# Kernel tuning notes

Measured on AMD Instinct MI355X. Metric: run time of the kernel, lower is better.

The kernel has to match this reference:

```python
import jax, jax.numpy as jnp
import numpy as np

EPS = 1e-5

def group_norm(x, gamma, beta):
    # GroupNorm(num_groups=1) on [N, C]: normalize across channels per row
    mu = jnp.mean(x, axis=-1, keepdims=True)
    var = jnp.mean(jnp.square(x - mu), axis=-1, keepdims=True)
    return (x - mu) * jax.lax.rsqrt(var + EPS) * gamma + beta

def setup_inputs() -> dict:
    key = jax.random.key(0)
    ks = jax.random.split(key, 20)
    Nc, Nt, E, D = 100_000, 100_000, 500_000, 128
    f32 = jnp.float32
    s_in, s_rp, s_ctx = 1.0 / np.sqrt(D), 0.5, 1.0 / np.sqrt(2 * D)
    return {
        "context_feat": jax.random.normal(ks[0], (Nc, D), dtype=f32),
        "target_feat": jax.random.normal(ks[1], (Nt, D), dtype=f32),
        "context_pose": jax.random.normal(ks[2], (Nc, 4), dtype=f32),
        "target_pose": jax.random.normal(ks[3], (Nt, 4), dtype=f32),
        "hi": jax.random.randint(ks[4], (E,), 0, Nc, dtype=jnp.int32),
        "wi": jax.random.randint(ks[5], (E,), 0, Nt, dtype=jnp.int32),
        # params (stored [in, out]; equals torch Linear with transposed weight)
        "W_in": jax.random.normal(ks[6], (D, D), dtype=f32) * s_in,
        "W_rp": jax.random.normal(ks[7], (4, D), dtype=f32) * s_rp,
        "b_rp": jnp.zeros((D,), dtype=f32),
        "W_ctx1": jax.random.normal(ks[8], (2 * D, D), dtype=f32) * s_ctx,
        "g_ctx": jnp.ones((D,), dtype=f32),
        "be_ctx": jnp.zeros((D,), dtype=f32),
        "W_ctx2": jax.random.normal(ks[9], (D, D), dtype=f32) * s_in,
        "g_n": jnp.ones((D,), dtype=f32),
        "be_n": jnp.zeros((D,), dtype=f32),
        "W_m1": jax.random.normal(ks[10], (D, D), dtype=f32) * s_in,
        "g_m1": jnp.ones((D,), dtype=f32),
        "be_m1": jnp.zeros((D,), dtype=f32),
        "W_m2": jax.random.normal(ks[11], (D, D), dtype=f32) * s_in,
        "g_m2": jnp.ones((D,), dtype=f32),
        "be_m2": jnp.zeros((D,), dtype=f32),
    }

def reference(context_feat, target_feat, context_pose, target_pose, hi, wi,
              W_in, W_rp, b_rp, W_ctx1, g_ctx, be_ctx, W_ctx2,
              g_n, be_n, W_m1, g_m1, be_m1, W_m2, g_m2, be_m2):
    # relpose MLP on gathered pose deltas: [E,4] -> [E,128]
    dist_feat = jax.nn.relu((context_pose[hi] - target_pose[wi]) @ W_rp + b_rp)
    # ctx branch: concat gathered context feats with relpose -> [E,256] -> [E,128]
    ctx = jnp.concatenate([context_feat[hi], dist_feat], axis=-1)
    ctx = jax.nn.relu(group_norm(ctx @ W_ctx1, g_ctx, be_ctx)) @ W_ctx2
    # scatter-add onto projected target feats
    identity = target_feat
    tf = target_feat @ W_in
    tf = tf.at[wi].add(ctx)
    tf = jax.nn.relu(group_norm(tf, g_n, be_n))
    # output MLP (Linear+GN+ReLU, Linear+GN)
    tf = jax.nn.relu(group_norm(tf @ W_m1, g_m1, be_m1))
    tf = group_norm(tf @ W_m2, g_m2, be_m2)
    return jax.nn.relu(tf + identity)
```

## Files before the change

### kernel.cpp

```cpp
#include <hip/hip_runtime.h>

typedef __bf16 bf16_t;
typedef bf16_t bf16x4 __attribute__((ext_vector_type(4)));
typedef bf16_t bf16x8 __attribute__((ext_vector_type(8)));
typedef float floatx4 __attribute__((ext_vector_type(4)));

#define EPSF 1e-5f
#define DEV static __device__ __forceinline__

__global__ __launch_bounds__(256) void k_prep(
    const float* __restrict__ W_in, const float* __restrict__ W_ctx1,
    const float* __restrict__ W_ctx2, const float* __restrict__ W_m1,
    const float* __restrict__ W_m2, bf16_t* __restrict__ sw)
{
    int idx = blockIdx.x * 256 + threadIdx.x;
    const float* W; int base, ks;
    if (idx < 16384)      { W = W_in;   base = 0;     ks = 2; }
    else if (idx < 49152) { W = W_ctx1; base = 16384; ks = 3; }
    else if (idx < 65536) { W = W_ctx2; base = 49152; ks = 2; }
    else if (idx < 81920) { W = W_m1;   base = 65536; ks = 2; }
    else                  { W = W_m2;   base = 81920; ks = 2; }
    int local = idx - base;
    int j = local & 7, l = (local >> 3) & 63, rest = local >> 9;
    int s = rest & ((1 << ks) - 1), t = rest >> ks;
    int k = s * 32 + (l >> 4) * 8 + j;
    int n = t * 16 + (l & 15);
    sw[idx] = (bf16_t)W[k * 128 + n];
}

DEV void gn_rows(floatx4* acc, int lane, const float* __restrict__ gamma,
                 const float* __restrict__ beta, bool do_relu)
{
    int m = lane & 15;
    float s1[4] = {0.f,0.f,0.f,0.f}, s2[4] = {0.f,0.f,0.f,0.f};
#pragma unroll
    for (int t = 0; t < 8; ++t)
#pragma unroll
        for (int rr = 0; rr < 4; ++rr) { float v = acc[t][rr]; s1[rr] += v; s2[rr] += v*v; }
#pragma unroll
    for (int mask = 1; mask <= 8; mask <<= 1)
#pragma unroll
        for (int rr = 0; rr < 4; ++rr) {
            s1[rr] += __shfl_xor(s1[rr], mask);
            s2[rr] += __shfl_xor(s2[rr], mask);
        }
    float mean[4], inv[4];
#pragma unroll
    for (int rr = 0; rr < 4; ++rr) {
        mean[rr] = s1[rr] * (1.f/128.f);
        float var = s2[rr] * (1.f/128.f) - mean[rr]*mean[rr];
        inv[rr] = rsqrtf(var + EPSF);
    }
#pragma unroll
    for (int t = 0; t < 8; ++t) {
        int n = t*16 + m;
        float ga = gamma[n], be = beta[n];
#pragma unroll
        for (int rr = 0; rr < 4; ++rr) {
            float v = (acc[t][rr] - mean[rr]) * inv[rr] * ga + be;
            acc[t][rr] = do_relu ? fmaxf(v, 0.f) : v;
        }
    }
}

__global__ __launch_bounds__(256) void k_count(const int* __restrict__ wi,
                                               int* __restrict__ cnt, int E)
{
    int e = blockIdx.x * 256 + threadIdx.x;
    if (e < E) atomicAdd(&cnt[wi[e]], 1);
}

__global__ __launch_bounds__(1024) void k_scan(const int* __restrict__ cnt,
                                               int* __restrict__ off, int Nt)
{
    __shared__ int wsum[16];
    __shared__ int s_carry;
    int tid = threadIdx.x, lane = tid & 63, wid = tid >> 6;
    if (tid == 0) s_carry = 0;
    __syncthreads();
    for (int bs = 0; bs < Nt; bs += 4096) {
        int i0 = bs + tid * 4;
        int v0 = 0, v1 = 0, v2 = 0, v3 = 0;
        if (i0 + 3 < Nt) {
            int4 v = *(const int4*)(cnt + i0);
            v0 = v.x; v1 = v.y; v2 = v.z; v3 = v.w;
        } else {
            if (i0     < Nt) v0 = cnt[i0];
            if (i0 + 1 < Nt) v1 = cnt[i0+1];
            if (i0 + 2 < Nt) v2 = cnt[i0+2];
            if (i0 + 3 < Nt) v3 = cnt[i0+3];
        }
        int tot = v0 + v1 + v2 + v3;
        int x = tot;
#pragma unroll
        for (int d = 1; d < 64; d <<= 1) {
            int y = __shfl_up(x, d);
            if (lane >= d) x += y;
        }
        if (lane == 63) wsum[wid] = x;
        __syncthreads();
        if (wid == 0) {
            int wv = (lane < 16) ? wsum[lane] : 0;
#pragma unroll
            for (int d = 1; d < 16; d <<= 1) {
                int y = __shfl_up(wv, d);
                if (lane >= d) wv += y;
            }
            if (lane < 16) wsum[lane] = wv;
        }
        __syncthreads();
        int ebase = s_carry + ((wid > 0) ? wsum[wid-1] : 0) + (x - tot);
        if (i0 + 3 < Nt) {
            *(int4*)(off + i0) = make_int4(ebase, ebase+v0, ebase+v0+v1, ebase+v0+v1+v2);
        } else {
            if (i0     < Nt) off[i0]   = ebase;
            if (i0 + 1 < Nt) off[i0+1] = ebase + v0;
            if (i0 + 2 < Nt) off[i0+2] = ebase + v0 + v1;
            if (i0 + 3 < Nt) off[i0+3] = ebase + v0 + v1 + v2;
        }
        __syncthreads();
        if (tid == 0) s_carry += wsum[15];
        __syncthreads();
    }
    if (tid == 0) off[Nt] = s_carry;
}

__global__ __launch_bounds__(256) void k_edge5(
    const float* __restrict__ cfeat, const float* __restrict__ cpose,
    const float* __restrict__ tpose, const int* __restrict__ hi,
    const int* __restrict__ wi, const float* __restrict__ W_rp,
    const float* __restrict__ b_rp, const float* __restrict__ g_ctx,
    const float* __restrict__ be_ctx, const bf16_t* __restrict__ swC1,
    const int* __restrict__ off, int* __restrict__ cur,
    bf16_t* __restrict__ hbuf, int E)
{
    __shared__ alignas(16) bf16_t sH[4][2176];
    int tid = threadIdx.x, lane = tid & 63, wave = tid >> 6;
    int tb = (blockIdx.x * 4 + wave) * 16;
    int r = lane & 15, g = lane >> 4;
    int e = min(tb + r, E - 1);
    int ci = hi[e], ti = wi[e];

    floatx4 acc[8];
#pragma unroll
    for (int t = 0; t < 8; ++t) acc[t] = (floatx4){0.f,0.f,0.f,0.f};

    const float4* cf = (const float4*)(cfeat + (size_t)ci * 128);
    float4 p[8];
#pragma unroll
    for (int s = 0; s < 4; ++s) {
        p[2*s]   = cf[s*8 + g*2];
        p[2*s+1] = cf[s*8 + g*2 + 1];
    }

    float4 cp = ((const float4*)cpose)[ci];
    float4 tp = ((const float4*)tpose)[ti];
    float d0 = cp.x - tp.x, d1 = cp.y - tp.y, d2 = cp.z - tp.z, d3 = cp.w - tp.w;
#pragma unroll
    for (int sp = 0; sp < 4; ++sp) {
        int k0 = sp * 32 + g * 8;
        const float4* w0 = (const float4*)(W_rp + k0);
        const float4* w1 = (const float4*)(W_rp + 128 + k0);
        const float4* w2 = (const float4*)(W_rp + 256 + k0);
        const float4* w3 = (const float4*)(W_rp + 384 + k0);
        const float4* bb = (const float4*)(b_rp + k0);
        float o0,o1,o2,o3,o4,o5,o6,o7;
        {
            float4 a0=w0[0], a1=w1[0], a2=w2[0], a3=w3[0], ab=bb[0];
            o0 = fmaxf(d0*a0.x + d1*a1.x + d2*a2.x + d3*a3.x + ab.x, 0.f);
            o1 = fmaxf(d0*a0.y + d1*a1.y + d2*a2.y + d3*a3.y + ab.y, 0.f);
            o2 = fmaxf(d0*a0.z + d1*a1.z + d2*a2.z + d3*a3.z + ab.z, 0.f);
            o3 = fmaxf(d0*a0.w + d1*a1.w + d2*a2.w + d3*a3.w + ab.w, 0.f);
        }
        {
            float4 a0=w0[1], a1=w1[1], a2=w2[1], a3=w3[1], ab=bb[1];
            o4 = fmaxf(d0*a0.x + d1*a1.x + d2*a2.x + d3*a3.x + ab.x, 0.f);
            o5 = fmaxf(d0*a0.y + d1*a1.y + d2*a2.y + d3*a3.y + ab.y, 0.f);
            o6 = fmaxf(d0*a0.z + d1*a1.z + d2*a2.z + d3*a3.z + ab.z, 0.f);
            o7 = fmaxf(d0*a0.w + d1*a1.w + d2*a2.w + d3*a3.w + ab.w, 0.f);
        }
        bf16x8 aF = { (bf16_t)o0, (bf16_t)o1, (bf16_t)o2, (bf16_t)o3,
                      (bf16_t)o4, (bf16_t)o5, (bf16_t)o6, (bf16_t)o7 };
        int s = 4 + sp;
#pragma unroll
        for (int t = 0; t < 8; ++t) {
            bf16x8 bF = *(const bf16x8*)&swC1[(size_t)((t*8 + s)*64 + lane)*8];
            acc[t] = __builtin_amdgcn_mfma_f32_16x16x32_bf16(aF, bF, acc[t], 0, 0, 0);
        }
    }
#pragma unroll
    for (int s = 0; s < 4; ++s) {
        float4 v0 = p[2*s], v1 = p[2*s+1];
        bf16x8 aF = { (bf16_t)v0.x, (bf16_t)v0.y, (bf16_t)v0.z, (bf16_t)v0.w,
                      (bf16_t)v1.x, (bf16_t)v1.y, (bf16_t)v1.z, (bf16_t)v1.w };
#pragma unroll
        for (int t = 0; t < 8; ++t) {
            bf16x8 bF = *(const bf16x8*)&swC1[(size_t)((t*8 + s)*64 + lane)*8];
            acc[t] = __builtin_amdgcn_mfma_f32_16x16x32_bf16(aF, bF, acc[t], 0, 0, 0);
        }
    }
    gn_rows(acc, lane, g_ctx, be_ctx, true);

#pragma unroll
    for (int t = 0; t < 8; ++t)
#pragma unroll
        for (int rr = 0; rr < 4; ++rr)
            sH[wave][(g*4 + rr)*136 + t*16 + r] = (bf16_t)acc[t][rr];

    int r2 = lane >> 2, c2 = lane & 3;
    int e2 = tb + r2;
    bool ev2 = e2 < E;
    int dst = 0;
    if (ev2 && c2 == 0) {
        int t2 = wi[e2];
        dst = off[t2] + atomicAdd(&cur[t2], 1);
    }
    dst = __shfl(dst, lane & ~3);
    if (ev2) {
        bf16_t* hp = hbuf + (size_t)dst * 128 + c2 * 32;
#pragma unroll
        for (int i = 0; i < 4; ++i)
            *(bf16x8*)(hp + i*8) = *(const bf16x8*)&sH[wave][r2*136 + c2*32 + i*8];
    }
}

__global__ __launch_bounds__(256) void k_out3(
    const float* __restrict__ tfeat, const bf16_t* __restrict__ hbuf,
    const int* __restrict__ off,
    const float* __restrict__ g_n, const float* __restrict__ be_n,
    const float* __restrict__ g_m1, const float* __restrict__ be_m1,
    const float* __restrict__ g_m2, const float* __restrict__ be_m2,
    const bf16_t* __restrict__ swIn, const bf16_t* __restrict__ swC2,
    const bf16_t* __restrict__ swM1, const bf16_t* __restrict__ swM2,
    float* __restrict__ out, int Nt)
{
    __shared__ alignas(16) bf16_t sB[4][2176];
    int tid = threadIdx.x, lane = tid & 63, wave = tid >> 6;
    int tb = (blockIdx.x*4 + wave)*16;
    int r = lane & 15, g = lane >> 4;
    int grow = tb + r;
    bool rv = grow < Nt;
    int rclamp = rv ? grow : (Nt - 1);

    const float4* cf = (const float4*)(tfeat + (size_t)rclamp * 128);
    float4 p[8];
#pragma unroll
    for (int s = 0; s < 4; ++s) {
        p[2*s]   = cf[s*8 + g*2];
        p[2*s+1] = cf[s*8 + g*2 + 1];
    }

    float sums[32];
#pragma unroll
    for (int i = 0; i < 32; ++i) sums[i] = 0.f;
    int jb = rv ? off[grow] : 0, je = rv ? off[grow+1] : 0;
    for (int jr = jb; jr < je; ++jr) {
        const bf16_t* hp = hbuf + (size_t)jr*128 + g*8;
#pragma unroll
        for (int s = 0; s < 4; ++s) {
            bf16x8 hv = *(const bf16x8*)(hp + s*32);
#pragma unroll
            for (int q = 0; q < 8; ++q) sums[s*8+q] += (float)hv[q];
        }
    }
#pragma unroll
    for (int s = 0; s < 4; ++s) {
        bf16x8 ah = { (bf16_t)sums[s*8+0], (bf16_t)sums[s*8+1],
                      (bf16_t)sums[s*8+2], (bf16_t)sums[s*8+3],
                      (bf16_t)sums[s*8+4], (bf16_t)sums[s*8+5],
                      (bf16_t)sums[s*8+6], (bf16_t)sums[s*8+7] };
        *(bf16x8*)&sB[wave][r*136 + s*32 + g*8] = ah;
    }

    floatx4 acc[8];
#pragma unroll
    for (int t = 0; t < 8; ++t) acc[t] = (floatx4){0.f,0.f,0.f,0.f};
#pragma unroll
    for (int s = 0; s < 4; ++s) {
        bf16x8 aH = *(const bf16x8*)&sB[wave][r*136 + s*32 + g*8];
#pragma unroll
        for (int t = 0; t < 8; ++t) {
            bf16x8 bF = *(const bf16x8*)&swC2[((t*4+s)*64 + lane)*8];
            acc[t] = __builtin_amdgcn_mfma_f32_16x16x32_bf16(aH, bF, acc[t], 0, 0, 0);
        }
        float4 v0 = p[2*s], v1 = p[2*s+1];
        bf16x8 aF = { (bf16_t)v0.x, (bf16_t)v0.y, (bf16_t)v0.z, (bf16_t)v0.w,
                      (bf16_t)v1.x, (bf16_t)v1.y, (bf16_t)v1.z, (bf16_t)v1.w };
#pragma unroll
        for (int t = 0; t < 8; ++t) {
            bf16x8 bF = *(const bf16x8*)&swIn[((t*4+s)*64 + lane)*8];
            acc[t] = __builtin_amdgcn_mfma_f32_16x16x32_bf16(aF, bF, acc[t], 0, 0, 0);
        }
    }
    gn_rows(acc, lane, g_n, be_n, true);

#pragma unroll
    for (int t = 0; t < 8; ++t)
#pragma unroll
        for (int rr = 0; rr < 4; ++rr)
            sB[wave][(g*4 + rr)*136 + t*16 + r] = (bf16_t)acc[t][rr];
#pragma unroll
    for (int t = 0; t < 8; ++t) acc[t] = (floatx4){0.f,0.f,0.f,0.f};
#pragma unroll
    for (int s = 0; s < 4; ++s) {
        bf16x8 aF = *(const bf16x8*)&sB[wave][r*136 + s*32 + g*8];
#pragma unroll
        for (int t = 0; t < 8; ++t) {
            bf16x8 bF = *(const bf16x8*)&swM1[((t*4+s)*64 + lane)*8];
            acc[t] = __builtin_amdgcn_mfma_f32_16x16x32_bf16(aF, bF, acc[t], 0, 0, 0);
        }
    }
    gn_rows(acc, lane, g_m1, be_m1, true);

#pragma unroll
    for (int t = 0; t < 8; ++t)
#pragma unroll
        for (int rr = 0; rr < 4; ++rr)
            sB[wave][(g*4 + rr)*136 + t*16 + r] = (bf16_t)acc[t][rr];
#pragma unroll
    for (int t = 0; t < 8; ++t) acc[t] = (floatx4){0.f,0.f,0.f,0.f};
#pragma unroll
    for (int s = 0; s < 4; ++s) {
        bf16x8 aF = *(const bf16x8*)&sB[wave][r*136 + s*32 + g*8];
#pragma unroll
        for (int t = 0; t < 8; ++t) {
            bf16x8 bF = *(const bf16x8*)&swM2[((t*4+s)*64 + lane)*8];
            acc[t] = __builtin_amdgcn_mfma_f32_16x16x32_bf16(aF, bF, acc[t], 0, 0, 0);
        }
    }
    gn_rows(acc, lane, g_m2, be_m2, false);

#pragma unroll
    for (int t = 0; t < 8; ++t) {
        int n = t*16 + r;
#pragma unroll
        for (int rr = 0; rr < 4; ++rr) {
            int row = tb + g*4 + rr;
            if (row < Nt) {
                float v = acc[t][rr] + tfeat[(size_t)row*128 + n];
                out[(size_t)row*128 + n] = fmaxf(v, 0.f);
            }
        }
    }
}

__global__ __launch_bounds__(256) void k_gemm_in(
    const float* __restrict__ tfeat, const bf16_t* __restrict__ swW,
    float* __restrict__ tf, int Nt)
{
    __shared__ alignas(16) bf16_t sA[4][2048];
    int tid = threadIdx.x, lane = tid & 63, wave = tid >> 6;

    int tb = (blockIdx.x * 4 + wave) * 16;
    int r = lane >> 2, cb = (lane & 3) * 32;
    int grow = tb + r;
    bool rv = grow < Nt;
    const float4* src = (const float4*)(tfeat + (size_t)(rv ? grow : 0) * 128 + cb);
#pragma unroll
    for (int i = 0; i < 8; ++i) {
        float4 v = rv ? src[i] : make_float4(0.f,0.f,0.f,0.f);
        int k = cb + 4*i;
        int s = k >> 5, q = (k >> 3) & 3, j = k & 7;
        bf16x4 pk = { (bf16_t)v.x, (bf16_t)v.y, (bf16_t)v.z, (bf16_t)v.w };
        *(bf16x4*)&sA[wave][(s*64 + q*16 + r)*8 + j] = pk;
    }
    __syncthreads();
    int m = lane & 15, g = lane >> 4;
    bf16x8 aF[4];
#pragma unroll
    for (int s = 0; s < 4; ++s) aF[s] = *(const bf16x8*)&sA[wave][(s*64 + lane)*8];
#pragma unroll
    for (int t = 0; t < 8; ++t) {
        floatx4 a = {0.f,0.f,0.f,0.f};
#pragma unroll
        for (int s = 0; s < 4; ++s) {
            bf16x8 bF = *(const bf16x8*)&swW[((t*4+s)*64 + lane)*8];
            a = __builtin_amdgcn_mfma_f32_16x16x32_bf16(aF[s], bF, a, 0, 0, 0);
        }
#pragma unroll
        for (int rr = 0; rr < 4; ++rr) {
            int row = tb + g*4 + rr;
            if (row < Nt) tf[(size_t)row*128 + t*16 + m] = a[rr];
        }
    }
}

__global__ __launch_bounds__(256) void k_edge_old(
    const float* __restrict__ cfeat, const float* __restrict__ cpose,
    const float* __restrict__ tpose, const int* __restrict__ hi,
    const int* __restrict__ wi, const float* __restrict__ W_rp,
    const float* __restrict__ b_rp, const float* __restrict__ g_ctx,
    const float* __restrict__ be_ctx, const bf16_t* __restrict__ swC1,
    const bf16_t* __restrict__ swC2, float* __restrict__ tf, int E)
{
    __shared__ alignas(16) bf16_t sA[4][4096];
    int tid = threadIdx.x, lane = tid & 63, wave = tid >> 6;

    int tb = (blockIdx.x * 4 + wave) * 16;
    int r = lane >> 2, cb = (lane & 3) * 32;
    int e = min(tb + r, E - 1);
    int ci = hi[e], ti = wi[e];
    const float4* src = (const float4*)(cfeat + (size_t)ci * 128 + cb);
#pragma unroll
    for (int i = 0; i < 8; ++i) {
        float4 v = src[i];
        int k = cb + 4*i;
        int s = k >> 5, q = (k >> 3) & 3, j = k & 7;
        bf16x4 pk = { (bf16_t)v.x, (bf16_t)v.y, (bf16_t)v.z, (bf16_t)v.w };
        *(bf16x4*)&sA[wave][(s*64 + q*16 + r)*8 + j] = pk;
    }
    float4 cp = ((const float4*)cpose)[ci];
    float4 tp = ((const float4*)tpose)[ti];
    float d0 = cp.x - tp.x, d1 = cp.y - tp.y, d2 = cp.z - tp.z, d3 = cp.w - tp.w;
#pragma unroll
    for (int i = 0; i < 8; ++i) {
        int cc = cb + 4*i;
        float4 w0 = *(const float4*)(W_rp + cc);
        float4 w1 = *(const float4*)(W_rp + 128 + cc);
        float4 w2 = *(const float4*)(W_rp + 256 + cc);
        float4 w3 = *(const float4*)(W_rp + 384 + cc);
        float4 bb = *(const float4*)(b_rp + cc);
        float o0 = fmaxf(d0*w0.x + d1*w1.x + d2*w2.x + d3*w3.x + bb.x, 0.f);
        float o1 = fmaxf(d0*w0.y + d1*w1.y + d2*w2.y + d3*w3.y + bb.y, 0.f);
        float o2 = fmaxf(d0*w0.z + d1*w1.z + d2*w2.z + d3*w3.z + bb.z, 0.f);
        float o3 = fmaxf(d0*w0.w + d1*w1.w + d2*w2.w + d3*w3.w + bb.w, 0.f);
        int k = 128 + cc;
        int s = k >> 5, q = (k >> 3) & 3, j = k & 7;
        bf16x4 pk = { (bf16_t)o0, (bf16_t)o1, (bf16_t)o2, (bf16_t)o3 };
        *(bf16x4*)&sA[wave][(s*64 + q*16 + r)*8 + j] = pk;
    }
    __syncthreads();

    int m = lane & 15, g = lane >> 4;
    bf16x8 aF[8];
#pragma unroll
    for (int s = 0; s < 8; ++s) aF[s] = *(const bf16x8*)&sA[wave][(s*64 + lane)*8];
    floatx4 acc[8];
#pragma unroll
    for (int t = 0; t < 8; ++t) {
        floatx4 a = {0.f,0.f,0.f,0.f};
#pragma unroll
        for (int s = 0; s < 8; ++s) {
            bf16x8 bF = *(const bf16x8*)&swC1[(size_t)((t*8+s)*64 + lane)*8];
            a = __builtin_amdgcn_mfma_f32_16x16x32_bf16(aF[s], bF, a, 0, 0, 0);
        }
        acc[t] = a;
    }
    gn_rows(acc, lane, g_ctx, be_ctx, true);
    __syncthreads();
#pragma unroll
    for (int t = 0; t < 8; ++t) {
        int n = t*16 + m;
        int s = n >> 5, q = (n >> 3) & 3, j = n & 7;
#pragma unroll
        for (int rr = 0; rr < 4; ++rr)
            sA[wave][(s*64 + q*16 + (g*4+rr))*8 + j] = (bf16_t)acc[t][rr];
    }
    __syncthreads();
    bf16x8 aF2[4];
#pragma unroll
    for (int s = 0; s < 4; ++s) aF2[s] = *(const bf16x8*)&sA[wave][(s*64 + lane)*8];
    int dstrow[4]; bool vald[4];
#pragma unroll
    for (int rr = 0; rr < 4; ++rr) {
        int ee = tb + g*4 + rr;
        vald[rr] = ee < E;
        dstrow[rr] = vald[rr] ? wi[ee] : 0;
    }
#pragma unroll
    for (int t = 0; t < 8; ++t) {
        floatx4 a = {0.f,0.f,0.f,0.f};
#pragma unroll
        for (int s = 0; s < 4; ++s) {
            bf16x8 bF = *(const bf16x8*)&swC2[((t*4+s)*64 + lane)*8];
            a = __builtin_amdgcn_mfma_f32_16x16x32_bf16(aF2[s], bF, a, 0, 0, 0);
        }
#pragma unroll
        for (int rr = 0; rr < 4; ++rr) {
            if (vald[rr])
                atomicAdd(&tf[(size_t)dstrow[rr]*128 + t*16 + m], a[rr]);
        }
    }
}

__global__ __launch_bounds__(256) void k_out_old(
    const float* __restrict__ tf, const float* __restrict__ identity,
    const float* __restrict__ g_n, const float* __restrict__ be_n,
    const float* __restrict__ g_m1, const float* __restrict__ be_m1,
    const float* __restrict__ g_m2, const float* __restrict__ be_m2,
    const bf16_t* __restrict__ swM1, const bf16_t* __restrict__ swM2,
    float* __restrict__ out, int Nt)
{
    __shared__ alignas(16) bf16_t sA[4][2048];
    int tid = threadIdx.x, lane = tid & 63, wave = tid >> 6;

    int tb = (blockIdx.x*4 + wave)*16;
    int r = lane >> 2, cb = (lane & 3)*32;
    int grow = tb + r;
    bool rv = grow < Nt;
    const float4* src = (const float4*)(tf + (size_t)(rv ? grow : 0)*128 + cb);
    float vals[32];
    float ls = 0.f, lq = 0.f;
#pragma unroll
    for (int i = 0; i < 8; ++i) {
        float4 v = rv ? src[i] : make_float4(0.f,0.f,0.f,0.f);
        vals[4*i+0]=v.x; vals[4*i+1]=v.y; vals[4*i+2]=v.z; vals[4*i+3]=v.w;
        ls += v.x+v.y+v.z+v.w;
        lq += v.x*v.x+v.y*v.y+v.z*v.z+v.w*v.w;
    }
    ls += __shfl_xor(ls,1); lq += __shfl_xor(lq,1);
    ls += __shfl_xor(ls,2); lq += __shfl_xor(lq,2);
    float mean = ls*(1.f/128.f);
    float inv = rsqrtf(lq*(1.f/128.f) - mean*mean + EPSF);
#pragma unroll
    for (int i = 0; i < 8; ++i) {
        int cc = cb + 4*i;
        float4 ga = *(const float4*)(g_n + cc);
        float4 be = *(const float4*)(be_n + cc);
        float o0 = fmaxf((vals[4*i+0]-mean)*inv*ga.x + be.x, 0.f);
        float o1 = fmaxf((vals[4*i+1]-mean)*inv*ga.y + be.y, 0.f);
        float o2 = fmaxf((vals[4*i+2]-mean)*inv*ga.z + be.z, 0.f);
        float o3 = fmaxf((vals[4*i+3]-mean)*inv*ga.w + be.w, 0.f);
        int s = cc >> 5, q = (cc >> 3) & 3, j = cc & 7;
        bf16x4 pk = { (bf16_t)o0, (bf16_t)o1, (bf16_t)o2, (bf16_t)o3 };
        *(bf16x4*)&sA[wave][(s*64 + q*16 + r)*8 + j] = pk;
    }
    __syncthreads();
    int m = lane & 15, g = lane >> 4;
    bf16x8 aF[4];
#pragma unroll
    for (int s = 0; s < 4; ++s) aF[s] = *(const bf16x8*)&sA[wave][(s*64 + lane)*8];
    floatx4 acc[8];
#pragma unroll
    for (int t = 0; t < 8; ++t) {
        floatx4 a = {0.f,0.f,0.f,0.f};
#pragma unroll
        for (int s = 0; s < 4; ++s) {
            bf16x8 bF = *(const bf16x8*)&swM1[((t*4+s)*64 + lane)*8];
            a = __builtin_amdgcn_mfma_f32_16x16x32_bf16(aF[s], bF, a, 0, 0, 0);
        }
        acc[t] = a;
    }
    gn_rows(acc, lane, g_m1, be_m1, true);
    __syncthreads();
#pragma unroll
    for (int t = 0; t < 8; ++t) {
        int n = t*16 + m;
        int s = n >> 5, q = (n >> 3) & 3, j = n & 7;
#pragma unroll
        for (int rr = 0; rr < 4; ++rr)
            sA[wave][(s*64 + q*16 + (g*4+rr))*8 + j] = (bf16_t)acc[t][rr];
    }
    __syncthreads();
#pragma unroll
    for (int s = 0; s < 4; ++s) aF[s] = *(const bf16x8*)&sA[wave][(s*64 + lane)*8];
#pragma unroll
    for (int t = 0; t < 8; ++t) {
        floatx4 a = {0.f,0.f,0.f,0.f};
#pragma unroll
        for (int s = 0; s < 4; ++s) {
            bf16x8 bF = *(const bf16x8*)&swM2[((t*4+s)*64 + lane)*8];
            a = __builtin_amdgcn_mfma_f32_16x16x32_bf16(aF[s], bF, a, 0, 0, 0);
        }
        acc[t] = a;
    }
    gn_rows(acc, lane, g_m2, be_m2, false);
#pragma unroll
    for (int t = 0; t < 8; ++t) {
        int n = t*16 + m;
#pragma unroll
        for (int rr = 0; rr < 4; ++rr) {
            int row = tb + g*4 + rr;
            if (row < Nt) {
                float v = acc[t][rr] + identity[(size_t)row*128 + n];
                out[(size_t)row*128 + n] = fmaxf(v, 0.f);
            }
        }
    }
}

extern "C" void kernel_launch(void* const* d_in, const int* in_sizes, int n_in,
                              void* d_out, int out_size, void* d_ws, size_t ws_size,
                              hipStream_t stream)
{
    const float* cfeat  = (const float*)d_in[0];
    const float* tfeat  = (const float*)d_in[1];
    const float* cpose  = (const float*)d_in[2];
    const float* tpose  = (const float*)d_in[3];
    const int*   hi     = (const int*)d_in[4];
    const int*   wi     = (const int*)d_in[5];
    const float* W_in   = (const float*)d_in[6];
    const float* W_rp   = (const float*)d_in[7];
    const float* b_rp   = (const float*)d_in[8];
    const float* W_ctx1 = (const float*)d_in[9];
    const float* g_ctx  = (const float*)d_in[10];
    const float* be_ctx = (const float*)d_in[11];
    const float* W_ctx2 = (const float*)d_in[12];
    const float* g_n    = (const float*)d_in[13];
    const float* be_n   = (const float*)d_in[14];
    const float* W_m1   = (const float*)d_in[15];
    const float* g_m1   = (const float*)d_in[16];
    const float* be_m1  = (const float*)d_in[17];
    const float* W_m2   = (const float*)d_in[18];
    const float* g_m2   = (const float*)d_in[19];
    const float* be_m2  = (const float*)d_in[20];

    int Nt = in_sizes[1] / 128;
    int E  = in_sizes[4];
    float* outp = (float*)d_out;

    char* base = (char*)d_ws;
    size_t o = 98304 * sizeof(bf16_t);
    o = (o + 255) & ~(size_t)255;
    size_t o_cnt = o; o += (size_t)Nt * 4;
    o = (o + 255) & ~(size_t)255;
    size_t o_off = o; o += ((size_t)Nt + 1) * 4;
    o = (o + 255) & ~(size_t)255;
    size_t o_cur = o; o += (size_t)Nt * 4;
    o = (o + 255) & ~(size_t)255;
    size_t o_h = o; o += (size_t)E * 128 * sizeof(bf16_t);

    if (ws_size >= o) {
        bf16_t* sw   = (bf16_t*)base;
        int*    cnt  = (int*)(base + o_cnt);
        int*    off  = (int*)(base + o_off);
        int*    cur  = (int*)(base + o_cur);
        bf16_t* hbuf = (bf16_t*)(base + o_h);
        bf16_t* swIn = sw;
        bf16_t* swC1 = sw + 16384;
        bf16_t* swC2 = sw + 49152;
        bf16_t* swM1 = sw + 65536;
        bf16_t* swM2 = sw + 81920;

        hipMemsetAsync(cnt, 0, (size_t)Nt * 4, stream);
        hipMemsetAsync(cur, 0, (size_t)Nt * 4, stream);
        k_prep<<<384, 256, 0, stream>>>(W_in, W_ctx1, W_ctx2, W_m1, W_m2, sw);
        k_count<<<(E + 255) / 256, 256, 0, stream>>>(wi, cnt, E);
        k_scan<<<1, 1024, 0, stream>>>(cnt, off, Nt);
        k_edge5<<<(E + 63) / 64, 256, 0, stream>>>(cfeat, cpose, tpose, hi, wi,
                                                   W_rp, b_rp, g_ctx, be_ctx,
                                                   swC1, off, cur, hbuf, E);
        k_out3<<<(Nt + 63) / 64, 256, 0, stream>>>(tfeat, hbuf, off,
                                                   g_n, be_n, g_m1, be_m1,
                                                   g_m2, be_m2,
                                                   swIn, swC2, swM1, swM2,
                                                   outp, Nt);
    } else {
        float*  tf = (float*)d_ws;
        bf16_t* sw = (bf16_t*)((char*)d_ws + (size_t)Nt * 128 * sizeof(float));
        bf16_t* swIn = sw;
        bf16_t* swC1 = sw + 16384;
        bf16_t* swC2 = sw + 49152;
        bf16_t* swM1 = sw + 65536;
        bf16_t* swM2 = sw + 81920;

        k_prep<<<384, 256, 0, stream>>>(W_in, W_ctx1, W_ctx2, W_m1, W_m2, sw);
        k_gemm_in<<<(Nt + 63) / 64, 256, 0, stream>>>(tfeat, swIn, tf, Nt);
        k_edge_old<<<(E + 63) / 64, 256, 0, stream>>>(cfeat, cpose, tpose, hi, wi,
                                                      W_rp, b_rp, g_ctx, be_ctx,
                                                      swC1, swC2, tf, E);
        k_out_old<<<(Nt + 63) / 64, 256, 0, stream>>>(tf, tfeat, g_n, be_n,
                                                      g_m1, be_m1, g_m2, be_m2,
                                                      swM1, swM2, outp, Nt);
    }
}
```

Before: 485.0 us.

## Process two 16-edge tiles per wave in edge kernel, reusing weight fragments

```diff
diff --git a/kernel.cpp b/kernel.cpp
--- a/kernel.cpp
+++ b/kernel.cpp
@@ -125,7 +125,7 @@
     if (tid == 0) off[Nt] = s_carry;
 }
 
-__global__ __launch_bounds__(256) void k_edge5(
+__global__ __launch_bounds__(256) void k_edge6(
     const float* __restrict__ cfeat, const float* __restrict__ cpose,
     const float* __restrict__ tpose, const int* __restrict__ hi,
     const int* __restrict__ wi, const float* __restrict__ W_rp,
@@ -136,26 +136,45 @@
 {
     __shared__ alignas(16) bf16_t sH[4][2176];
     int tid = threadIdx.x, lane = tid & 63, wave = tid >> 6;
-    int tb = (blockIdx.x * 4 + wave) * 16;
+    int tb = (blockIdx.x * 4 + wave) * 32;
     int r = lane & 15, g = lane >> 4;
-    int e = min(tb + r, E - 1);
-    int ci = hi[e], ti = wi[e];
-
-    floatx4 acc[8];
-#pragma unroll
-    for (int t = 0; t < 8; ++t) acc[t] = (floatx4){0.f,0.f,0.f,0.f};
-
-    const float4* cf = (const float4*)(cfeat + (size_t)ci * 128);
-    float4 p[8];
-#pragma unroll
-    for (int s = 0; s < 4; ++s) {
-        p[2*s]   = cf[s*8 + g*2];
-        p[2*s+1] = cf[s*8 + g*2 + 1];
-    }
-
-    float4 cp = ((const float4*)cpose)[ci];
-    float4 tp = ((const float4*)tpose)[ti];
-    float d0 = cp.x - tp.x, d1 = cp.y - tp.y, d2 = cp.z - tp.z, d3 = cp.w - tp.w;
+    int e0 = min(tb + r, E - 1);
+    int e1 = min(tb + 16 + r, E - 1);
+    int ci0 = hi[e0], ti0 = wi[e0];
+    int ci1 = hi[e1], ti1 = wi[e1];
+
+    int r2 = lane >> 2, c2 = lane & 3;
+    int ea = tb + r2, eb = tb + 16 + r2;
+    bool eva = ea < E, evb = eb < E;
+    int dst0 = 0, dst1 = 0;
+    if (c2 == 0) {
+        if (eva) { int t2 = wi[ea]; dst0 = off[t2] + atomicAdd(&cur[t2], 1); }
+        if (evb) { int t2 = wi[eb]; dst1 = off[t2] + atomicAdd(&cur[t2], 1); }
+    }
+    dst0 = __shfl(dst0, lane & ~3);
+    dst1 = __shfl(dst1, lane & ~3);
+
+    floatx4 acc0[8], acc1[8];
+#pragma unroll
+    for (int t = 0; t < 8; ++t) {
+        acc0[t] = (floatx4){0.f,0.f,0.f,0.f};
+        acc1[t] = (floatx4){0.f,0.f,0.f,0.f};
+    }
+
+    const float4* cf0 = (const float4*)(cfeat + (size_t)ci0 * 128);
+    const float4* cf1 = (const float4*)(cfeat + (size_t)ci1 * 128);
+    float4 t0b[2][2], t1b[2][2];
+    t0b[0][0] = cf0[g*2];     t0b[0][1] = cf0[g*2 + 1];
+    t1b[0][0] = cf1[g*2];     t1b[0][1] = cf1[g*2 + 1];
+    t0b[1][0] = cf0[8 + g*2]; t0b[1][1] = cf0[8 + g*2 + 1];
+    t1b[1][0] = cf1[8 + g*2]; t1b[1][1] = cf1[8 + g*2 + 1];
+
+    float4 cp0 = ((const float4*)cpose)[ci0];
+    float4 tp0 = ((const float4*)tpose)[ti0];
+    float4 cp1 = ((const float4*)cpose)[ci1];
+    float4 tp1 = ((const float4*)tpose)[ti1];
+    float d00 = cp0.x - tp0.x, d01 = cp0.y - tp0.y, d02 = cp0.z - tp0.z, d03 = cp0.w - tp0.w;
+    float d10 = cp1.x - tp1.x, d11 = cp1.y - tp1.y, d12 = cp1.z - tp1.z, d13 = cp1.w - tp1.w;
 #pragma unroll
     for (int sp = 0; sp < 4; ++sp) {
         int k0 = sp * 32 + g * 8;
@@ -164,60 +183,71 @@
         const float4* w2 = (const float4*)(W_rp + 256 + k0);
         const float4* w3 = (const float4*)(W_rp + 384 + k0);
         const float4* bb = (const float4*)(b_rp + k0);
-        float o0,o1,o2,o3,o4,o5,o6,o7;
-        {
-            float4 a0=w0[0], a1=w1[0], a2=w2[0], a3=w3[0], ab=bb[0];
-            o0 = fmaxf(d0*a0.x + d1*a1.x + d2*a2.x + d3*a3.x + ab.x, 0.f);
-            o1 = fmaxf(d0*a0.y + d1*a1.y + d2*a2.y + d3*a3.y + ab.y, 0.f);
-            o2 = fmaxf(d0*a0.z + d1*a1.z + d2*a2.z + d3*a3.z + ab.z, 0.f);
-            o3 = fmaxf(d0*a0.w + d1*a1.w + d2*a2.w + d3*a3.w + ab.w, 0.f);
-        }
-        {
-            float4 a0=w0[1], a1=w1[1], a2=w2[1], a3=w3[1], ab=bb[1];
-            o4 = fmaxf(d0*a0.x + d1*a1.x + d2*a2.x + d3*a3.x + ab.x, 0.f);
-            o5 = fmaxf(d0*a0.y + d1*a1.y + d2*a2.y + d3*a3.y + ab.y, 0.f);
-            o6 = fmaxf(d0*a0.z + d1*a1.z + d2*a2.z + d3*a3.z + ab.z, 0.f);
-            o7 = fmaxf(d0*a0.w + d1*a1.w + d2*a2.w + d3*a3.w + ab.w, 0.f);
-        }
-        bf16x8 aF = { (bf16_t)o0, (bf16_t)o1, (bf16_t)o2, (bf16_t)o3,
-                      (bf16_t)o4, (bf16_t)o5, (bf16_t)o6, (bf16_t)o7 };
+        float o0[8], o1[8];
+#pragma unroll
+        for (int h = 0; h < 2; ++h) {
+            float4 a0 = w0[h], a1 = w1[h], a2 = w2[h], a3 = w3[h], ab = bb[h];
+            o0[4*h+0] = fmaxf(d00*a0.x + d01*a1.x + d02*a2.x + d03*a3.x + ab.x, 0.f);
+            o0[4*h+1] = fmaxf(d00*a0.y + d01*a1.y + d02*a2.y + d03*a3.y + ab.y, 0.f);
+            o0[4*h+2] = fmaxf(d00*a0.z + d01*a1.z + d02*a2.z + d03*a3.z + ab.z, 0.f);
+            o0[4*h+3] = fmaxf(d00*a0.w + d01*a1.w + d02*a2.w + d03*a3.w + ab.w, 0.f);
+            o1[4*h+0] = fmaxf(d10*a0.x + d11*a1.x + d12*a2.x + d13*a3.x + ab.x, 0.f);
+            o1[4*h+1] = fmaxf(d10*a0.y + d11*a1.y + d12*a2.y + d13*a3.y + ab.y, 0.f);
+            o1[4*h+2] = fmaxf(d10*a0.z + d11*a1.z + d12*a2.z + d13*a3.z + ab.z, 0.f);
+            o1[4*h+3] = fmaxf(d10*a0.w + d11*a1.w + d12*a2.w + d13*a3.w + ab.w, 0.f);
+        }
+        bf16x8 aF0 = { (bf16_t)o0[0], (bf16_t)o0[1], (bf16_t)o0[2], (bf16_t)o0[3],
+                       (bf16_t)o0[4], (bf16_t)o0[5], (bf16_t)o0[6], (bf16_t)o0[7] };
+        bf16x8 aF1 = { (bf16_t)o1[0], (bf16_t)o1[1], (bf16_t)o1[2], (bf16_t)o1[3],
+                       (bf16_t)o1[4], (bf16_t)o1[5], (bf16_t)o1[6], (bf16_t)o1[7] };
         int s = 4 + sp;
 #pragma unroll
         for (int t = 0; t < 8; ++t) {
             bf16x8 bF = *(const bf16x8*)&swC1[(size_t)((t*8 + s)*64 + lane)*8];
-            acc[t] = __builtin_amdgcn_mfma_f32_16x16x32_bf16(aF, bF, acc[t], 0, 0, 0);
+            acc0[t] = __builtin_amdgcn_mfma_f32_16x16x32_bf16(aF0, bF, acc0[t], 0, 0, 0);
+            acc1[t] = __builtin_amdgcn_mfma_f32_16x16x32_bf16(aF1, bF, acc1[t], 0, 0, 0);
         }
     }
 #pragma unroll
     for (int s = 0; s < 4; ++s) {
-        float4 v0 = p[2*s], v1 = p[2*s+1];
-        bf16x8 aF = { (bf16_t)v0.x, (bf16_t)v0.y, (bf16_t)v0.z, (bf16_t)v0.w,
-                      (bf16_t)v1.x, (bf16_t)v1.y, (bf16_t)v1.z, (bf16_t)v1.w };
+        float4 v00 = t0b[s & 1][0], v01 = t0b[s & 1][1];
+        float4 v10 = t1b[s & 1][0], v11 = t1b[s & 1][1];
+        if (s < 2) {
+            t0b[s & 1][0] = cf0[(s+2)*8 + g*2]; t0b[s & 1][1] = cf0[(s+2)*8 + g*2 + 1];
+            t1b[s & 1][0] = cf1[(s+2)*8 + g*2]; t1b[s & 1][1] = cf1[(s+2)*8 + g*2 + 1];
+        }
+        bf16x8 aF0 = { (bf16_t)v00.x, (bf16_t)v00.y, (bf16_t)v00.z, (bf16_t)v00.w,
+                       (bf16_t)v01.x, (bf16_t)v01.y, (bf16_t)v01.z, (bf16_t)v01.w };
+        bf16x8 aF1 = { (bf16_t)v10.x, (bf16_t)v10.y, (bf16_t)v10.z, (bf16_t)v10.w,
+                       (bf16_t)v11.x, (bf16_t)v11.y, (bf16_t)v11.z, (bf16_t)v11.w };
 #pragma unroll
         for (int t = 0; t < 8; ++t) {
             bf16x8 bF = *(const bf16x8*)&swC1[(size_t)((t*8 + s)*64 + lane)*8];
-            acc[t] = __builtin_amdgcn_mfma_f32_16x16x32_bf16(aF, bF, acc[t], 0, 0, 0);
-        }
-    }
-    gn_rows(acc, lane, g_ctx, be_ctx, true);
-
+            acc0[t] = __builtin_amdgcn_mfma_f32_16x16x32_bf16(aF0, bF, acc0[t], 0, 0, 0);
+            acc1[t] = __builtin_amdgcn_mfma_f32_16x16x32_bf16(aF1, bF, acc1[t], 0, 0, 0);
+        }
+    }
+
+    gn_rows(acc0, lane, g_ctx, be_ctx, true);
 #pragma unroll
     for (int t = 0; t < 8; ++t)
 #pragma unroll
         for (int rr = 0; rr < 4; ++rr)
-            sH[wave][(g*4 + rr)*136 + t*16 + r] = (bf16_t)acc[t][rr];
-
-    int r2 = lane >> 2, c2 = lane & 3;
-    int e2 = tb + r2;
-    bool ev2 = e2 < E;
-    int dst = 0;
-    if (ev2 && c2 == 0) {
-        int t2 = wi[e2];
-        dst = off[t2] + atomicAdd(&cur[t2], 1);
-    }
-    dst = __shfl(dst, lane & ~3);
-    if (ev2) {
-        bf16_t* hp = hbuf + (size_t)dst * 128 + c2 * 32;
+            sH[wave][(g*4 + rr)*136 + t*16 + r] = (bf16_t)acc0[t][rr];
+    if (eva) {
+        bf16_t* hp = hbuf + (size_t)dst0 * 128 + c2 * 32;
+#pragma unroll
+        for (int i = 0; i < 4; ++i)
+            *(bf16x8*)(hp + i*8) = *(const bf16x8*)&sH[wave][r2*136 + c2*32 + i*8];
+    }
+    gn_rows(acc1, lane, g_ctx, be_ctx, true);
+#pragma unroll
+    for (int t = 0; t < 8; ++t)
+#pragma unroll
+        for (int rr = 0; rr < 4; ++rr)
+            sH[wave][(g*4 + rr)*136 + t*16 + r] = (bf16_t)acc1[t][rr];
+    if (evb) {
+        bf16_t* hp = hbuf + (size_t)dst1 * 128 + c2 * 32;
 #pragma unroll
         for (int i = 0; i < 4; ++i)
             *(bf16x8*)(hp + i*8) = *(const bf16x8*)&sH[wave][r2*136 + c2*32 + i*8];
@@ -637,9 +667,9 @@
         k_prep<<<384, 256, 0, stream>>>(W_in, W_ctx1, W_ctx2, W_m1, W_m2, sw);
         k_count<<<(E + 255) / 256, 256, 0, stream>>>(wi, cnt, E);
         k_scan<<<1, 1024, 0, stream>>>(cnt, off, Nt);
-        k_edge5<<<(E + 63) / 64, 256, 0, stream>>>(cfeat, cpose, tpose, hi, wi,
-                                                   W_rp, b_rp, g_ctx, be_ctx,
-                                                   swC1, off, cur, hbuf, E);
+        k_edge6<<<(E + 127) / 128, 256, 0, stream>>>(cfeat, cpose, tpose, hi, wi,
+                                                     W_rp, b_rp, g_ctx, be_ctx,
+                                                     swC1, off, cur, hbuf, E);
         k_out3<<<(Nt + 63) / 64, 256, 0, stream>>>(tfeat, hbuf, off,
                                                    g_n, be_n, g_m1, be_m1,
                                                    g_m2, be_m2,
```

Result: no change. 480.4 us (-0.9%).

## Process edges in context-index sorted order for gather locality

Applied to the files above, without the earlier changes.

```diff
diff --git a/kernel.cpp b/kernel.cpp
--- a/kernel.cpp
+++ b/kernel.cpp
@@ -63,32 +63,32 @@
     }
 }
 
-__global__ __launch_bounds__(256) void k_count(const int* __restrict__ wi,
+__global__ __launch_bounds__(256) void k_count(const int* __restrict__ idxs,
                                                int* __restrict__ cnt, int E)
 {
     int e = blockIdx.x * 256 + threadIdx.x;
-    if (e < E) atomicAdd(&cnt[wi[e]], 1);
+    if (e < E) atomicAdd(&cnt[idxs[e]], 1);
 }
 
 __global__ __launch_bounds__(1024) void k_scan(const int* __restrict__ cnt,
-                                               int* __restrict__ off, int Nt)
+                                               int* __restrict__ off, int N)
 {
     __shared__ int wsum[16];
     __shared__ int s_carry;
     int tid = threadIdx.x, lane = tid & 63, wid = tid >> 6;
     if (tid == 0) s_carry = 0;
     __syncthreads();
-    for (int bs = 0; bs < Nt; bs += 4096) {
+    for (int bs = 0; bs < N; bs += 4096) {
         int i0 = bs + tid * 4;
         int v0 = 0, v1 = 0, v2 = 0, v3 = 0;
-        if (i0 + 3 < Nt) {
+        if (i0 + 3 < N) {
             int4 v = *(const int4*)(cnt + i0);
             v0 = v.x; v1 = v.y; v2 = v.z; v3 = v.w;
         } else {
-            if (i0     < Nt) v0 = cnt[i0];
-            if (i0 + 1 < Nt) v1 = cnt[i0+1];
-            if (i0 + 2 < Nt) v2 = cnt[i0+2];
-            if (i0 + 3 < Nt) v3 = cnt[i0+3];
+            if (i0     < N) v0 = cnt[i0];
+            if (i0 + 1 < N) v1 = cnt[i0+1];
+            if (i0 + 2 < N) v2 = cnt[i0+2];
+            if (i0 + 3 < N) v3 = cnt[i0+3];
         }
         int tot = v0 + v1 + v2 + v3;
         int x = tot;
@@ -110,25 +110,39 @@
         }
         __syncthreads();
         int ebase = s_carry + ((wid > 0) ? wsum[wid-1] : 0) + (x - tot);
-        if (i0 + 3 < Nt) {
+        if (i0 + 3 < N) {
             *(int4*)(off + i0) = make_int4(ebase, ebase+v0, ebase+v0+v1, ebase+v0+v1+v2);
         } else {
-            if (i0     < Nt) off[i0]   = ebase;
-            if (i0 + 1 < Nt) off[i0+1] = ebase + v0;
-            if (i0 + 2 < Nt) off[i0+2] = ebase + v0 + v1;
-            if (i0 + 3 < Nt) off[i0+3] = ebase + v0 + v1 + v2;
+            if (i0     < N) off[i0]   = ebase;
+            if (i0 + 1 < N) off[i0+1] = ebase + v0;
+            if (i0 + 2 < N) off[i0+2] = ebase + v0 + v1;
+            if (i0 + 3 < N) off[i0+3] = ebase + v0 + v1 + v2;
         }
         __syncthreads();
         if (tid == 0) s_carry += wsum[15];
         __syncthreads();
     }
-    if (tid == 0) off[Nt] = s_carry;
-}
-
-__global__ __launch_bounds__(256) void k_edge5(
+    if (tid == 0) off[N] = s_carry;
+}
+
+__global__ __launch_bounds__(256) void k_scatter(const int* __restrict__ hi,
+                                                 const int* __restrict__ off_h,
+                                                 int* __restrict__ cur_h,
+                                                 int* __restrict__ eidx, int E)
+{
+    int e = blockIdx.x * 256 + threadIdx.x;
+    if (e < E) {
+        int h = hi[e];
+        int p = off_h[h] + atomicAdd(&cur_h[h], 1);
+        eidx[p] = e;
+    }
+}
+
+__global__ __launch_bounds__(256) void k_edge7(
     const float* __restrict__ cfeat, const float* __restrict__ cpose,
     const float* __restrict__ tpose, const int* __restrict__ hi,
-    const int* __restrict__ wi, const float* __restrict__ W_rp,
+    const int* __restrict__ wi, const int* __restrict__ eidx,
+    const float* __restrict__ W_rp,
     const float* __restrict__ b_rp, const float* __restrict__ g_ctx,
     const float* __restrict__ be_ctx, const bf16_t* __restrict__ swC1,
     const int* __restrict__ off, int* __restrict__ cur,
@@ -138,8 +152,16 @@
     int tid = threadIdx.x, lane = tid & 63, wave = tid >> 6;
     int tb = (blockIdx.x * 4 + wave) * 16;
     int r = lane & 15, g = lane >> 4;
-    int e = min(tb + r, E - 1);
+    int pos = min(tb + r, E - 1);
+    int e = eidx[pos];
     int ci = hi[e], ti = wi[e];
+
+    int r2 = lane >> 2, c2 = lane & 3;
+    bool ev2 = (tb + r2) < E;
+    int ti2 = __shfl(ti, r2);
+    int dst = 0;
+    if (ev2 && c2 == 0) dst = off[ti2] + atomicAdd(&cur[ti2], 1);
+    dst = __shfl(dst, lane & ~3);
 
     floatx4 acc[8];
 #pragma unroll
@@ -207,15 +229,6 @@
         for (int rr = 0; rr < 4; ++rr)
             sH[wave][(g*4 + rr)*136 + t*16 + r] = (bf16_t)acc[t][rr];
 
-    int r2 = lane >> 2, c2 = lane & 3;
-    int e2 = tb + r2;
-    bool ev2 = e2 < E;
-    int dst = 0;
-    if (ev2 && c2 == 0) {
-        int t2 = wi[e2];
-        dst = off[t2] + atomicAdd(&cur[t2], 1);
-    }
-    dst = __shfl(dst, lane & ~3);
     if (ev2) {
         bf16_t* hp = hbuf + (size_t)dst * 128 + c2 * 32;
 #pragma unroll
@@ -606,6 +619,7 @@
     const float* be_m2  = (const float*)d_in[20];
 
     int Nt = in_sizes[1] / 128;
+    int Nc = in_sizes[0] / 128;
     int E  = in_sizes[4];
     float* outp = (float*)d_out;
 
@@ -618,14 +632,26 @@
     o = (o + 255) & ~(size_t)255;
     size_t o_cur = o; o += (size_t)Nt * 4;
     o = (o + 255) & ~(size_t)255;
+    size_t o_cnth = o; o += (size_t)Nc * 4;
+    o = (o + 255) & ~(size_t)255;
+    size_t o_offh = o; o += ((size_t)Nc + 1) * 4;
+    o = (o + 255) & ~(size_t)255;
+    size_t o_curh = o; o += (size_t)Nc * 4;
+    o = (o + 255) & ~(size_t)255;
+    size_t o_eidx = o; o += (size_t)E * 4;
+    o = (o + 255) & ~(size_t)255;
     size_t o_h = o; o += (size_t)E * 128 * sizeof(bf16_t);
 
     if (ws_size >= o) {
-        bf16_t* sw   = (bf16_t*)base;
-        int*    cnt  = (int*)(base + o_cnt);
-        int*    off  = (int*)(base + o_off);
-        int*    cur  = (int*)(base + o_cur);
-        bf16_t* hbuf = (bf16_t*)(base + o_h);
+        bf16_t* sw    = (bf16_t*)base;
+        int*    cnt   = (int*)(base + o_cnt);
+        int*    off   = (int*)(base + o_off);
+        int*    cur   = (int*)(base + o_cur);
+        int*    cnth  = (int*)(base + o_cnth);
+        int*    offh  = (int*)(base + o_offh);
+        int*    curh  = (int*)(base + o_curh);
+        int*    eidx  = (int*)(base + o_eidx);
+        bf16_t* hbuf  = (bf16_t*)(base + o_h);
         bf16_t* swIn = sw;
         bf16_t* swC1 = sw + 16384;
         bf16_t* swC2 = sw + 49152;
@@ -634,11 +660,16 @@
 
         hipMemsetAsync(cnt, 0, (size_t)Nt * 4, stream);
         hipMemsetAsync(cur, 0, (size_t)Nt * 4, stream);
+        hipMemsetAsync(cnth, 0, (size_t)Nc * 4, stream);
+        hipMemsetAsync(curh, 0, (size_t)Nc * 4, stream);
         k_prep<<<384, 256, 0, stream>>>(W_in, W_ctx1, W_ctx2, W_m1, W_m2, sw);
         k_count<<<(E + 255) / 256, 256, 0, stream>>>(wi, cnt, E);
         k_scan<<<1, 1024, 0, stream>>>(cnt, off, Nt);
-        k_edge5<<<(E + 63) / 64, 256, 0, stream>>>(cfeat, cpose, tpose, hi, wi,
-                                                   W_rp, b_rp, g_ctx, be_ctx,
+        k_count<<<(E + 255) / 256, 256, 0, stream>>>(hi, cnth, E);
+        k_scan<<<1, 1024, 0, stream>>>(cnth, offh, Nc);
+        k_scatter<<<(E + 255) / 256, 256, 0, stream>>>(hi, offh, curh, eidx, E);
+        k_edge7<<<(E + 63) / 64, 256, 0, stream>>>(cfeat, cpose, tpose, hi, wi,
+                                                   eidx, W_rp, b_rp, g_ctx, be_ctx,
                                                    swC1, off, cur, hbuf, E);
         k_out3<<<(Nt + 63) / 64, 256, 0, stream>>>(tfeat, hbuf, off,
                                                    g_n, be_n, g_m1, be_m1,
```

Measured after the change: 557.0 us. 1.15x slower.
